# Kernel optimization log

Hardware: AMD Instinct MI355X
Metric: run time of the kernel (lower is better)

Reference implementation:

```python
import jax, jax.numpy as jnp
import numpy as np

DIM = 64
NUM_HEADS = 4
SIGMA_RATIO = 1.0


def setup_inputs() -> dict:
    key = jax.random.key(0)
    ks = jax.random.split(key, 10)
    d = DIM
    s = 0.02
    return {
        "x": jax.random.normal(ks[0], (2, d, 64, 64), dtype=jnp.float32),
        "qkv_w": jax.random.normal(ks[1], (3 * d, d), dtype=jnp.float32) * s,
        "qkv_b": jnp.zeros((3 * d,), dtype=jnp.float32),
        "proj_w": jax.random.normal(ks[2], (d, d), dtype=jnp.float32) * s,
        "proj_b": jnp.zeros((d,), dtype=jnp.float32),
        "g1_w": jax.random.normal(ks[3], (16, 1), dtype=jnp.float32) * 0.5,
        "g1_b": jnp.zeros((16,), dtype=jnp.float32),
        "g2_w": jax.random.normal(ks[4], (NUM_HEADS, 16), dtype=jnp.float32) * 0.5,
        "g2_b": jnp.zeros((NUM_HEADS,), dtype=jnp.float32),
    }


def reference(x, qkv_w, qkv_b, proj_w, proj_b, g1_w, g1_b, g2_w, g2_b):
    B, C, H, W = x.shape
    nh = NUM_HEADS
    hd = C // nh
    N = H * W
    scale = hd ** -0.5

    # edge strength |x[i]-x[i-1]| summed over channels, replicate-padded
    diff_h = jnp.abs(x[:, :, :, 1:] - x[:, :, :, :-1]).sum(axis=1)  # [B,H,W-1]
    diff_v = jnp.abs(x[:, :, 1:, :] - x[:, :, :-1, :]).sum(axis=1)  # [B,H-1,W]
    edge_h = jnp.pad(diff_h, ((0, 0), (0, 0), (0, 1)), mode="edge")
    edge_v = jnp.pad(diff_v, ((0, 0), (0, 1), (0, 0)), mode="edge")
    es = (edge_h + edge_v)[..., None]  # [B,H,W,1]

    # gate MLP: Linear(1,16) -> GELU(exact) -> Linear(16,nh) -> sigmoid
    h1 = jax.nn.gelu(es @ g1_w.T + g1_b, approximate=False)
    gate = jax.nn.sigmoid(h1 @ g2_w.T + g2_b)  # [B,H,W,nh]

    x_seq = x.transpose(0, 2, 3, 1).reshape(B, N, C)
    qkv = (x_seq @ qkv_w.T + qkv_b).reshape(B, N, 3, nh, hd)
    qkv = qkv.transpose(2, 0, 3, 1, 4)  # [3,B,nh,N,hd]
    q, k, v = qkv[0], qkv[1], qkv[2]

    attn = jax.nn.softmax(jnp.einsum("bhnd,bhmd->bhnm", q, k) * scale, axis=-1)

    gate_sender = gate.reshape(B, N, nh).transpose(0, 2, 1)  # [B,nh,N]
    gate_sender = (1.0 - gate_sender * SIGMA_RATIO * 0.1)[..., None]  # [B,nh,N,1]
    attn = attn * gate_sender
    attn = attn / (attn.sum(axis=-1, keepdims=True) + 1e-8)

    out = jnp.einsum("bhnm,bhmd->bnhd", attn, v).reshape(B, N, C)
    out = out @ proj_w.T + proj_b
    return out.reshape(B, H, W, C).transpose(0, 3, 1, 2)
```

## Files before the change

kernel.cpp:

```cpp
#include <hip/hip_runtime.h>
#include <cstdint>


namespace {
constexpr int B  = 2;
constexpr int C  = 64;
constexpr int NH = 4;
constexpr int HD = 16;
constexpr int N  = 4096;
constexpr int MSA = 4;

constexpr size_t QKV1     = (size_t)B * NH * N * HD;
constexpr size_t KB_OFF   = QKV1;
constexpr size_t VT_OFF   = 2 * QKV1;
constexpr size_t PO_OFF_U = 3 * QKV1;
constexpr size_t PO_SZ    = (size_t)B * NH * MSA * N * HD;
constexpr size_t PL_OFF_F = (PO_OFF_U + PO_SZ) / 2;
constexpr float QSCALE = 0.36067376022224085f;
}

typedef short bf16x8 __attribute__((ext_vector_type(8)));
typedef float f32x16 __attribute__((ext_vector_type(16)));
typedef int   i32x4  __attribute__((ext_vector_type(4)));

__device__ __forceinline__ unsigned short f2bf(float f) {
  unsigned u = __float_as_uint(f);
  u = (u + 0x7fffu + ((u >> 16) & 1u)) >> 16;
  return (unsigned short)u;
}
__device__ __forceinline__ int cvtpk(float lo, float hi) {
  int r;
  asm("v_cvt_pk_bf16_f32 %0, %1, %2" : "=v"(r) : "v"(lo), "v"(hi));
  return r;
}
__device__ __forceinline__ float fexp2(float x) {
#if __has_builtin(__builtin_amdgcn_exp2f)
  return __builtin_amdgcn_exp2f(x);
#else
  float r;
  asm("v_exp_f32 %0, %1" : "=v"(r) : "v"(x));
  return r;
#endif
}
__device__ __forceinline__ float frcp(float x) {
#if __has_builtin(__builtin_amdgcn_rcpf)
  return __builtin_amdgcn_rcpf(x);
#else
  float r;
  asm("v_rcp_f32 %0, %1" : "=v"(r) : "v"(x));
  return r;
#endif
}
__device__ __forceinline__ void plswap(int a, int b, int h, int& x, int& y) {
#if __has_builtin(__builtin_amdgcn_permlane32_swap)
  (void)h;
  auto r = __builtin_amdgcn_permlane32_swap(a, b, false, false);
  x = r[0]; y = r[1];
#else
  const int ea = __shfl_xor(a, 32), eb = __shfl_xor(b, 32);
  x = h ? eb : a;
  y = h ? b : ea;
#endif
}

__global__ __launch_bounds__(256) void qkv_mfma_kernel(
    const float* __restrict__ x, const float* __restrict__ w,
    const float* __restrict__ bias, unsigned short* __restrict__ qb,
    unsigned short* __restrict__ kb, unsigned short* __restrict__ vtb) {
  __shared__ char wl[64 * 128];
  __shared__ char tl[4 * 2048];
  const int tid = threadIdx.x;
  const int lane = tid & 63, wid = tid >> 6;
  const int l31 = lane & 31, h = lane >> 5;
  const int nw = wid >> 1, jw = wid & 1;
  const int b = blockIdx.y, n0 = blockIdx.x * 64, z = blockIdx.z;

#pragma unroll
  for (int k = 0; k < 8; ++k) {
    const int p = tid + k * 256;
    const int j = p >> 5, c2 = (p & 31) * 2;
    const float2 wv = *(const float2*)(w + ((size_t)z * 64 + j) * 64 + c2);
    *(int*)(wl + j * 128 + ((2 * c2) ^ ((j & 7) << 4))) = cvtpk(wv.x, wv.y);
  }

  const int nA = n0 + nw * 32 + l31;
  bf16x8 af[4];
#pragma unroll
  for (int kk = 0; kk < 4; ++kk) {
    float e[8];
#pragma unroll
    for (int i = 0; i < 8; ++i)
      e[i] = x[((size_t)b * C + kk * 16 + h * 8 + i) * N + nA];
    i32x4 pk = {cvtpk(e[0], e[1]), cvtpk(e[2], e[3]),
                cvtpk(e[4], e[5]), cvtpk(e[6], e[7])};
    af[kk] = __builtin_bit_cast(bf16x8, pk);
  }
  __syncthreads();

  const int j = jw * 32 + l31;
  f32x16 acc = {};
#pragma unroll
  for (int kk = 0; kk < 4; ++kk) {
    bf16x8 bf =
        *(const bf16x8*)(wl + j * 128 + ((kk * 32 + h * 16) ^ ((j & 7) << 4)));
    acc = __builtin_amdgcn_mfma_f32_32x32x16_bf16(af[kk], bf, acc, 0, 0, 0);
  }
  const float bj = bias[z * 64 + j];
  char* myt = tl + wid * 2048;
  const int mt32 = (n0 >> 5) + nw;

  if (z < 2) {
    const float sc = (z == 0) ? QSCALE : 1.0f;
#pragma unroll
    for (int r = 0; r < 16; ++r) {
      const int n = (r & 3) + 8 * (r >> 2) + 4 * h;
      *(unsigned short*)(myt + n * 64 + l31 * 2) = f2bf((acc[r] + bj) * sc);
    }
#pragma unroll
    for (int u = 0; u < 2; ++u) {
      const int chunk = lane * 2 + u;
      const int n = chunk >> 2, c = chunk & 3;
      const uint4 vv = *(const uint4*)(myt + n * 64 + c * 16);
      const int jj = jw * 32 + c * 8;
      const int hh = jj >> 4, half = (jj >> 3) & 1;
      const int bh = b * NH + hh;
      if (z == 0) {
        *(uint4*)(qb + ((size_t)bh * N + n0 + nw * 32 + n) * HD + half * 8) = vv;
      } else {
        const size_t ck = (size_t)bh * 8192 + (size_t)mt32 * 64 + half * 32 + n;
        *(uint4*)(kb + ck * 8) = vv;
      }
    }
  } else {
#pragma unroll
    for (int p = 0; p < 8; ++p) {
      const int r = 2 * p;
      const int n = (r & 3) + 8 * (r >> 2) + 4 * h;
      *(int*)(myt + l31 * 64 + n * 2) = cvtpk(acc[r] + bj, acc[r + 1] + bj);
    }
#pragma unroll
    for (int u = 0; u < 2; ++u) {
      const int chunk = lane * 2 + u;
      const int jj = chunk >> 2, c = chunk & 3;
      const uint4 vv = *(const uint4*)(myt + jj * 64 + c * 16);
      const int vj = jw * 32 + jj;
      const int hh = vj >> 4, hd = vj & 15;
      const size_t ck =
          (((size_t)(b * NH + hh) * 128 + mt32) * 4 + c) * 16 + hd;
      *(uint4*)(vtb + ck * 8) = vv;
    }
  }
}

__global__ __launch_bounds__(256, 4) void attn_mfma_kernel(
    const unsigned short* __restrict__ qb, const unsigned short* __restrict__ kb,
    const unsigned short* __restrict__ vtb, unsigned short* __restrict__ part_o,
    float* __restrict__ part_l) {
  __shared__ char tl[4 * 1024];
  const int tid  = threadIdx.x;
  const int lane = tid & 63;
  const int wid  = tid >> 6;
  const int l31  = lane & 31;
  const int h    = lane >> 5;
  const int bh = blockIdx.z;
  const int ms = blockIdx.y;
  const int q0 = blockIdx.x * 128 + wid * 32;
  const int m0 = ms * (N / MSA);
  constexpr int NIT = (N / MSA) / 32;

  bf16x8 qf;
  {
    const uint4 qv =
        *(const uint4*)(qb + (((size_t)bh * N) + q0 + l31) * HD + h * 8);
    qf = __builtin_bit_cast(bf16x8, qv);
  }
  const unsigned short* kp =
      kb + ((size_t)bh * 8192 + (size_t)(m0 >> 5) * 64 + h * 32 + l31) * 8;
  const unsigned short* vp =
      vtb + ((((size_t)bh * 128 + (m0 >> 5)) * 4 + h) * 16 + l31) * 8;

  const int onef = (l31 == HD) ? 0x3F803F80 : 0;
  const i32x4 onev = {onef, onef, onef, onef};
  const bf16x8 vcst = __builtin_bit_cast(bf16x8, onev);

  f32x16 acc = {};
#pragma unroll 8
  for (int cc = 0; cc < NIT; ++cc) {
    bf16x8 kf = *(const bf16x8*)(kp + (size_t)cc * 512);
    f32x16 zv = {};
    f32x16 st = __builtin_amdgcn_mfma_f32_32x32x16_bf16(kf, qf, zv, 0, 0, 0);
    bf16x8 vf1, vf2;
    if (l31 < HD) {
      vf1 = *(const bf16x8*)(vp + (size_t)cc * 512);
      vf2 = *(const bf16x8*)(vp + (size_t)cc * 512 + 256);
    } else {
      vf1 = vcst;
      vf2 = vcst;
    }
    int dw[8];
#pragma unroll
    for (int jj = 0; jj < 8; ++jj)
      dw[jj] = cvtpk(fexp2(st[2 * jj]), fexp2(st[2 * jj + 1]));
    int w0, w1, w2, w3, w4, w5, w6, w7;
    plswap(dw[0], dw[2], h, w0, w2);
    plswap(dw[1], dw[3], h, w1, w3);
    plswap(dw[4], dw[6], h, w4, w6);
    plswap(dw[5], dw[7], h, w5, w7);
    const i32x4 a1 = {w0, w1, w2, w3};
    const i32x4 a2 = {w4, w5, w6, w7};
    acc = __builtin_amdgcn_mfma_f32_32x32x16_bf16(
        __builtin_bit_cast(bf16x8, a1), vf1, acc, 0, 0, 0);
    acc = __builtin_amdgcn_mfma_f32_32x32x16_bf16(
        __builtin_bit_cast(bf16x8, a2), vf2, acc, 0, 0, 0);
  }

  const size_t pbase = ((size_t)bh * MSA + ms) * N + q0;
  if (l31 == HD) {
#pragma unroll
    for (int r = 0; r < 16; ++r)
      part_l[pbase + (r & 3) + 8 * (r >> 2) + 4 * h] = acc[r];
  }
  char* myt = tl + wid * 1024;
  if (l31 < HD) {
#pragma unroll
    for (int r = 0; r < 16; ++r) {
      const int q = (r & 3) + 8 * (r >> 2) + 4 * h;
      *(unsigned short*)(myt + q * 32 + l31 * 2) = f2bf(acc[r]);
    }
  }
  __syncthreads();
  const int qr = lane >> 1, half = lane & 1;
  const uint4 vv = *(const uint4*)(myt + qr * 32 + half * 16);
  *(uint4*)(part_o + (pbase + qr) * HD + half * 8) = vv;
}

__global__ __launch_bounds__(128) void proj_mfma_kernel(
    const unsigned short* __restrict__ part_o, const float* __restrict__ part_l,
    const float* __restrict__ pw, const float* __restrict__ pb,
    float* __restrict__ out) {
  __shared__ char al[32 * 128];
  __shared__ char bl[64 * 128];
  __shared__ char tl[2 * 4096];
  __shared__ float linv[128];
  const int tid = threadIdx.x;
  const int lane = tid & 63, wid = tid >> 6;
  const int l31 = lane & 31, h = lane >> 5;
  const int b = blockIdx.y, n0 = blockIdx.x * 32;

  {
    const int hh = tid >> 5, n = tid & 31;
    const size_t base = ((size_t)(b * NH + hh) * MSA) * N + n0 + n;
    float l = 0.f;
#pragma unroll
    for (int ms = 0; ms < MSA; ++ms) l += part_l[base + (size_t)ms * N];
    linv[tid] = frcp(l);
  }
#pragma unroll
  for (int k = 0; k < 16; ++k) {
    const int p = tid + k * 128;
    const int cR = p >> 5, d2 = (p & 31) * 2;
    const float2 wv = *(const float2*)(pw + cR * 64 + d2);
    *(int*)(bl + cR * 128 + ((2 * d2) ^ ((cR & 7) << 4))) = cvtpk(wv.x, wv.y);
  }
  __syncthreads();

#pragma unroll
  for (int u = 0; u < 2; ++u) {
    const int chunk = tid * 2 + u;
    const int hh = chunk >> 6, half = (chunk >> 5) & 1, n = chunk & 31;
    const unsigned short* src =
        part_o + (((size_t)(b * NH + hh) * MSA) * N + n0 + n) * HD + half * 8;
    float s[8] = {0.f, 0.f, 0.f, 0.f, 0.f, 0.f, 0.f, 0.f};
#pragma unroll
    for (int ms = 0; ms < MSA; ++ms) {
      const uint4 v = *(const uint4*)(src + (size_t)ms * N * HD);
      const unsigned uu[4] = {v.x, v.y, v.z, v.w};
#pragma unroll
      for (int q = 0; q < 4; ++q) {
        s[2 * q]     += __uint_as_float(uu[q] << 16);
        s[2 * q + 1] += __uint_as_float(uu[q] & 0xffff0000u);
      }
    }
    const float iv = linv[hh * 32 + n];
    const i32x4 pk = {cvtpk(s[0] * iv, s[1] * iv), cvtpk(s[2] * iv, s[3] * iv),
                      cvtpk(s[4] * iv, s[5] * iv), cvtpk(s[6] * iv, s[7] * iv)};
    const int d = hh * 16 + half * 8;
    *(i32x4*)(al + n * 128 + ((2 * d) ^ ((n & 7) << 4))) = pk;
  }
  __syncthreads();

  bf16x8 af[4];
#pragma unroll
  for (int kk = 0; kk < 4; ++kk)
    af[kk] = *(const bf16x8*)(al + l31 * 128 +
                              ((kk * 32 + h * 16) ^ ((l31 & 7) << 4)));
  const int c = wid * 32 + l31;
  f32x16 acc = {};
#pragma unroll
  for (int kk = 0; kk < 4; ++kk) {
    bf16x8 bf =
        *(const bf16x8*)(bl + c * 128 + ((kk * 32 + h * 16) ^ ((c & 7) << 4)));
    acc = __builtin_amdgcn_mfma_f32_32x32x16_bf16(af[kk], bf, acc, 0, 0, 0);
  }
  const float bc = pb[c];

  char* myt = tl + wid * 4096;
#pragma unroll
  for (int p = 0; p < 8; ++p) {
    const int r = 2 * p;
    const int n = (r & 3) + 8 * (r >> 2) + 4 * h;
    *(float2*)(myt + l31 * 128 + n * 4) =
        make_float2(acc[r] + bc, acc[r + 1] + bc);
  }
  __syncthreads();
#pragma unroll
  for (int u = 0; u < 4; ++u) {
    const int chunk = lane * 4 + u;
    const int cc = chunk >> 3, cq = chunk & 7;
    const float4 vv = *(const float4*)(myt + cc * 128 + cq * 16);
    *(float4*)(out + ((size_t)b * C + wid * 32 + cc) * N + n0 + cq * 4) = vv;
  }
}

extern "C" void kernel_launch(void* const* d_in, const int* in_sizes, int n_in,
                              void* d_out, int out_size, void* d_ws, size_t ws_size,
                              hipStream_t stream) {
  const float* x      = (const float*)d_in[0];
  const float* qkv_w  = (const float*)d_in[1];
  const float* qkv_b  = (const float*)d_in[2];
  const float* proj_w = (const float*)d_in[3];
  const float* proj_b = (const float*)d_in[4];
  unsigned short* qb     = (unsigned short*)d_ws;
  unsigned short* kb     = qb + KB_OFF;
  unsigned short* vtb    = qb + VT_OFF;
  unsigned short* part_o = qb + PO_OFF_U;
  float* part_l = (float*)d_ws + PL_OFF_F;
  float* out = (float*)d_out;

  qkv_mfma_kernel<<<dim3(N / 64, B, 3), 256, 0, stream>>>(
      x, qkv_w, qkv_b, qb, kb, vtb);
  attn_mfma_kernel<<<dim3(N / 128, MSA, B * NH), 256, 0, stream>>>(
      qb, kb, vtb, part_o, part_l);
  proj_mfma_kernel<<<dim3(N / 32, B), 128, 0, stream>>>(
      part_o, part_l, proj_w, proj_b, out);
}
```

Before: 37.40 us.

## Stage K tiles in double-buffered LDS and raise key-split to eight

K fragments for each 128-key tile are now loaded cooperatively into double-buffered shared memory and shared across the four waves, with the next tile prefetched into registers while the current one is consumed. Previously each wave read K directly from global memory. The key-axis split grows from four to eight partitions, and the occupancy hint goes from four to five blocks per CU. This adds a block-wide barrier per tile and doubles the partial-output traffic the projection kernel must reduce.

```diff
diff --git a/kernel.cpp b/kernel.cpp
--- a/kernel.cpp
+++ b/kernel.cpp
@@ -8,7 +8,7 @@
 constexpr int NH = 4;
 constexpr int HD = 16;
 constexpr int N  = 4096;
-constexpr int MSA = 4;
+constexpr int MSA = 8;
 
 constexpr size_t QKV1     = (size_t)B * NH * N * HD;
 constexpr size_t KB_OFF   = QKV1;
@@ -152,11 +152,11 @@
   }
 }
 
-__global__ __launch_bounds__(256, 4) void attn_mfma_kernel(
+__global__ __launch_bounds__(256, 5) void attn_mfma_kernel(
     const unsigned short* __restrict__ qb, const unsigned short* __restrict__ kb,
     const unsigned short* __restrict__ vtb, unsigned short* __restrict__ part_o,
     float* __restrict__ part_l) {
-  __shared__ char tl[4 * 1024];
+  __shared__ char ldsb[2 * 4096];
   const int tid  = threadIdx.x;
   const int lane = tid & 63;
   const int wid  = tid >> 6;
@@ -166,7 +166,7 @@
   const int ms = blockIdx.y;
   const int q0 = blockIdx.x * 128 + wid * 32;
   const int m0 = ms * (N / MSA);
-  constexpr int NIT = (N / MSA) / 32;
+  constexpr int NT = (N / MSA) / 128;
 
   bf16x8 qf;
   {
@@ -174,44 +174,61 @@
         *(const uint4*)(qb + (((size_t)bh * N) + q0 + l31) * HD + h * 8);
     qf = __builtin_bit_cast(bf16x8, qv);
   }
-  const unsigned short* kp =
-      kb + ((size_t)bh * 8192 + (size_t)(m0 >> 5) * 64 + h * 32 + l31) * 8;
+  const unsigned short* kgp = kb + ((size_t)bh * 8192 + (size_t)(m0 >> 5) * 64) * 8;
   const unsigned short* vp =
       vtb + ((((size_t)bh * 128 + (m0 >> 5)) * 4 + h) * 16 + l31) * 8;
+
+  {
+    const uint4 k0 = *(const uint4*)(kgp + (size_t)tid * 8);
+    *(uint4*)(ldsb + tid * 16) = k0;
+  }
+  __syncthreads();
 
   const int onef = (l31 == HD) ? 0x3F803F80 : 0;
   const i32x4 onev = {onef, onef, onef, onef};
   const bf16x8 vcst = __builtin_bit_cast(bf16x8, onev);
 
   f32x16 acc = {};
-#pragma unroll 8
-  for (int cc = 0; cc < NIT; ++cc) {
-    bf16x8 kf = *(const bf16x8*)(kp + (size_t)cc * 512);
-    f32x16 zv = {};
-    f32x16 st = __builtin_amdgcn_mfma_f32_32x32x16_bf16(kf, qf, zv, 0, 0, 0);
-    bf16x8 vf1, vf2;
-    if (l31 < HD) {
-      vf1 = *(const bf16x8*)(vp + (size_t)cc * 512);
-      vf2 = *(const bf16x8*)(vp + (size_t)cc * 512 + 256);
-    } else {
-      vf1 = vcst;
-      vf2 = vcst;
-    }
-    int dw[8];
-#pragma unroll
-    for (int jj = 0; jj < 8; ++jj)
-      dw[jj] = cvtpk(fexp2(st[2 * jj]), fexp2(st[2 * jj + 1]));
-    int w0, w1, w2, w3, w4, w5, w6, w7;
-    plswap(dw[0], dw[2], h, w0, w2);
-    plswap(dw[1], dw[3], h, w1, w3);
-    plswap(dw[4], dw[6], h, w4, w6);
-    plswap(dw[5], dw[7], h, w5, w7);
-    const i32x4 a1 = {w0, w1, w2, w3};
-    const i32x4 a2 = {w4, w5, w6, w7};
-    acc = __builtin_amdgcn_mfma_f32_32x32x16_bf16(
-        __builtin_bit_cast(bf16x8, a1), vf1, acc, 0, 0, 0);
-    acc = __builtin_amdgcn_mfma_f32_32x32x16_bf16(
-        __builtin_bit_cast(bf16x8, a2), vf2, acc, 0, 0, 0);
+  int cur = 0;
+  for (int t = 0; t < NT; ++t) {
+    uint4 k0{};
+    const bool pre = (t + 1 < NT);
+    if (pre)
+      k0 = *(const uint4*)(kgp + ((size_t)(t + 1) * 256 + tid) * 8);
+    const char* kbase = ldsb + cur * 4096;
+#pragma unroll
+    for (int cc = 0; cc < 4; ++cc) {
+      const int it = t * 4 + cc;
+      bf16x8 kf = *(const bf16x8*)(kbase + (cc * 64 + h * 32 + l31) * 16);
+      f32x16 zv = {};
+      f32x16 st = __builtin_amdgcn_mfma_f32_32x32x16_bf16(kf, qf, zv, 0, 0, 0);
+      bf16x8 vf1, vf2;
+      if (l31 < HD) {
+        vf1 = *(const bf16x8*)(vp + (size_t)it * 512);
+        vf2 = *(const bf16x8*)(vp + (size_t)it * 512 + 256);
+      } else {
+        vf1 = vcst;
+        vf2 = vcst;
+      }
+      int dw[8];
+#pragma unroll
+      for (int jj = 0; jj < 8; ++jj)
+        dw[jj] = cvtpk(fexp2(st[2 * jj]), fexp2(st[2 * jj + 1]));
+      int w0, w1, w2, w3, w4, w5, w6, w7;
+      plswap(dw[0], dw[2], h, w0, w2);
+      plswap(dw[1], dw[3], h, w1, w3);
+      plswap(dw[4], dw[6], h, w4, w6);
+      plswap(dw[5], dw[7], h, w5, w7);
+      const i32x4 a1 = {w0, w1, w2, w3};
+      const i32x4 a2 = {w4, w5, w6, w7};
+      acc = __builtin_amdgcn_mfma_f32_32x32x16_bf16(
+          __builtin_bit_cast(bf16x8, a1), vf1, acc, 0, 0, 0);
+      acc = __builtin_amdgcn_mfma_f32_32x32x16_bf16(
+          __builtin_bit_cast(bf16x8, a2), vf2, acc, 0, 0, 0);
+    }
+    if (pre) *(uint4*)(ldsb + (cur ^ 1) * 4096 + tid * 16) = k0;
+    __syncthreads();
+    cur ^= 1;
   }
 
   const size_t pbase = ((size_t)bh * MSA + ms) * N + q0;
@@ -220,7 +237,7 @@
     for (int r = 0; r < 16; ++r)
       part_l[pbase + (r & 3) + 8 * (r >> 2) + 4 * h] = acc[r];
   }
-  char* myt = tl + wid * 1024;
+  char* myt = ldsb + wid * 1024;
   if (l31 < HD) {
 #pragma unroll
     for (int r = 0; r < 16; ++r) {
```

Result: slower. 38.97 us (+4.2%).
